# Kernel optimization log

Measured on AMD Instinct MI355X. Metric: run time of the kernel, lower is better.

The kernel has to match this reference:

```python
import jax, jax.numpy as jnp
import numpy as np

N_NODES = 100000
N_EDGES = 1600000
IN_F, HID, OUT_F = 128, 128, 64
BN_EPS = 1e-5


def _sage_conv(x, src, dst, W_l, b_l, W_r, n_nodes):
    # PyG SAGEConv (aggr='mean', root_weight=True):
    #   out_i = W_l @ mean_{j in N(i)} x_j + b_l + W_r @ x_i
    msg = x[src]                                             # [E, d] gather
    agg = jax.ops.segment_sum(msg, dst, num_segments=n_nodes)  # [N, d]
    deg = jax.ops.segment_sum(jnp.ones((src.shape[0],), x.dtype), dst,
                              num_segments=n_nodes)          # [N]
    agg = agg / jnp.clip(deg, 1.0)[:, None]
    return agg @ W_l.T + b_l + x @ W_r.T


def setup_inputs() -> dict:
    key = jax.random.key(0)
    ks = jax.random.split(key, 10)
    x = jax.random.normal(ks[0], (N_NODES, IN_F), dtype=jnp.float32)
    edge_index = jax.random.randint(ks[1], (2, N_EDGES), 0, N_NODES, dtype=jnp.int64)
    s = 0.05
    return {
        "x": x,
        "edge_index": edge_index,
        "W1_l": jax.random.normal(ks[2], (HID, IN_F), dtype=jnp.float32) * s,
        "b1": jnp.zeros((HID,), jnp.float32),
        "W1_r": jax.random.normal(ks[3], (HID, IN_F), dtype=jnp.float32) * s,
        "bn_gamma": jnp.ones((HID,), jnp.float32),
        "bn_beta": jnp.zeros((HID,), jnp.float32),
        "bn_mean": jax.random.normal(ks[4], (HID,), dtype=jnp.float32) * 0.1,
        "bn_var": jnp.ones((HID,), jnp.float32),
        "W2_l": jax.random.normal(ks[5], (OUT_F, HID), dtype=jnp.float32) * s,
        "b2": jnp.zeros((OUT_F,), jnp.float32),
        "W2_r": jax.random.normal(ks[6], (OUT_F, HID), dtype=jnp.float32) * s,
    }


def reference(x, edge_index, W1_l, b1, W1_r, bn_gamma, bn_beta, bn_mean, bn_var,
              W2_l, b2, W2_r):
    src, dst = edge_index[0], edge_index[1]
    n = x.shape[0]
    # eval mode: dropout = identity
    h = _sage_conv(x, src, dst, W1_l, b1, W1_r, n)            # [N, HID]
    # BatchNorm1d (eval, running stats)
    h = (h - bn_mean) * jax.lax.rsqrt(bn_var + BN_EPS) * bn_gamma + bn_beta
    h = jax.nn.relu(h)
    return _sage_conv(h, src, dst, W2_l, b2, W2_r, n)         # [N, OUT_F]
```

## Files before the change

### kernel.cpp

```cpp
#include <hip/hip_runtime.h>

#define FEAT 128
#define BN_EPS 1e-5f
#define CSTRIDE 16

typedef __attribute__((ext_vector_type(8))) short s8frag;
typedef __attribute__((ext_vector_type(4))) float f4frag;

union FragU { uint4 u; s8frag v; };

__device__ __forceinline__ unsigned short f2bf(float f) {
    unsigned u = __float_as_uint(f);
    unsigned r = (u + 0x7fffu + ((u >> 16) & 1u)) >> 16;
    return (unsigned short)r;
}
__device__ __forceinline__ void unpack2(unsigned d, float& lo, float& hi) {
    lo = __uint_as_float(d << 16);
    hi = __uint_as_float(d & 0xffff0000u);
}
__device__ __forceinline__ void acc8(float* acc, uint4 d) {
    float l, h;
    unpack2(d.x, l, h); acc[0] += l; acc[1] += h;
    unpack2(d.y, l, h); acc[2] += l; acc[3] += h;
    unpack2(d.z, l, h); acc[4] += l; acc[5] += h;
    unpack2(d.w, l, h); acc[6] += l; acc[7] += h;
}

__global__ __launch_bounds__(256) void front_kernel(
    const int* __restrict__ dst, int E, int Tc,
    unsigned* __restrict__ degc, unsigned char* __restrict__ rank8,
    const float* __restrict__ x, unsigned short* __restrict__ xb, int total8,
    const float* __restrict__ W1l, const float* __restrict__ W1r,
    const float* __restrict__ W2l, const float* __restrict__ W2r,
    const float* __restrict__ b1, const float* __restrict__ g,
    const float* __restrict__ bt, const float* __restrict__ mu,
    const float* __restrict__ var, const float* __restrict__ b2,
    unsigned short* __restrict__ Wb1, unsigned short* __restrict__ Wb2,
    float* __restrict__ bnsc, float* __restrict__ bnsh, float* __restrict__ cb2)
{
    int tid = blockIdx.x * 256 + threadIdx.x;
    if (tid < Tc) {
        int base = tid * 8;
        if (base + 8 <= E) {
            int4 d0 = *(const int4*)(dst + base);
            int4 d1 = *(const int4*)(dst + base + 4);
            unsigned r0 = atomicAdd(&degc[(size_t)d0.x * CSTRIDE], 1u);
            unsigned r1 = atomicAdd(&degc[(size_t)d0.y * CSTRIDE], 1u);
            unsigned r2 = atomicAdd(&degc[(size_t)d0.z * CSTRIDE], 1u);
            unsigned r3 = atomicAdd(&degc[(size_t)d0.w * CSTRIDE], 1u);
            unsigned r4 = atomicAdd(&degc[(size_t)d1.x * CSTRIDE], 1u);
            unsigned r5 = atomicAdd(&degc[(size_t)d1.y * CSTRIDE], 1u);
            unsigned r6 = atomicAdd(&degc[(size_t)d1.z * CSTRIDE], 1u);
            unsigned r7 = atomicAdd(&degc[(size_t)d1.w * CSTRIDE], 1u);
            unsigned p0 = (r0 & 255u) | ((r1 & 255u) << 8) | ((r2 & 255u) << 16) | ((r3 & 255u) << 24);
            unsigned p1 = (r4 & 255u) | ((r5 & 255u) << 8) | ((r6 & 255u) << 16) | ((r7 & 255u) << 24);
            ((unsigned*)rank8)[tid * 2]     = p0;
            ((unsigned*)rank8)[tid * 2 + 1] = p1;
        } else {
            for (int e = base; e < E; e++)
                rank8[e] = (unsigned char)atomicAdd(&degc[(size_t)dst[e] * CSTRIDE], 1u);
        }
    } else if (tid < Tc + total8) {
        int t = tid - Tc;
        const float4* src = (const float4*)(x) + (size_t)t * 2;
        float4 a = src[0], b = src[1];
        uint4 o;
        o.x = f2bf(a.x) | ((unsigned)f2bf(a.y) << 16);
        o.y = f2bf(a.z) | ((unsigned)f2bf(a.w) << 16);
        o.z = f2bf(b.x) | ((unsigned)f2bf(b.y) << 16);
        o.w = f2bf(b.z) | ((unsigned)f2bf(b.w) << 16);
        ((uint4*)xb)[t] = o;
    } else {
        int idx = tid - Tc - total8;
        if (idx < 128 * 256) {
            int n = idx >> 8, k = idx & 255;
            float w = (k < 128) ? W1l[n * 128 + k] : W1r[n * 128 + (k - 128)];
            Wb1[idx] = f2bf(w);
        }
        if (idx < 128 * 128) {
            int n = idx >> 7, k = idx & 127;
            float w = (n < 64) ? W2l[n * 128 + k] : W2r[(n - 64) * 128 + k];
            Wb2[idx] = f2bf(w);
        }
        if (idx < 128) {
            float sc = rsqrtf(var[idx] + BN_EPS) * g[idx];
            bnsc[idx] = sc;
            bnsh[idx] = sc * (b1[idx] - mu[idx]) + bt[idx];
            cb2[idx] = (idx < 64) ? 0.f : b2[idx - 64];
        }
    }
}

__global__ void scan_block(const unsigned* __restrict__ degc, unsigned* __restrict__ excl,
                           unsigned* __restrict__ partials, int N) {
    __shared__ unsigned buf[256];
    int i = blockIdx.x * 256 + threadIdx.x;
    unsigned v = (i < N) ? degc[(size_t)i * CSTRIDE] : 0u;
    buf[threadIdx.x] = v;
    __syncthreads();
    for (int off = 1; off < 256; off <<= 1) {
        unsigned t = (threadIdx.x >= (unsigned)off) ? buf[threadIdx.x - off] : 0u;
        __syncthreads();
        buf[threadIdx.x] += t;
        __syncthreads();
    }
    if (i < N) excl[i] = buf[threadIdx.x] - v;
    if (threadIdx.x == 255) partials[blockIdx.x] = buf[255];
}

__global__ void scan_finish(unsigned* __restrict__ row_start,
                            const unsigned* __restrict__ partials, int N, int E) {
    __shared__ unsigned red[256];
    int b = blockIdx.x;
    unsigned s = 0;
    for (int t = threadIdx.x; t < b; t += 256) s += partials[t];
    red[threadIdx.x] = s;
    __syncthreads();
    for (int off = 128; off > 0; off >>= 1) {
        if ((int)threadIdx.x < off) red[threadIdx.x] += red[threadIdx.x + off];
        __syncthreads();
    }
    unsigned base = red[0];
    int i = b * 256 + threadIdx.x;
    if (i < N) row_start[i] += base;
    if (i == 0) row_start[N] = (unsigned)E;
}

__global__ void fill_csr(const int* __restrict__ src, const int* __restrict__ dst, int E,
                         const unsigned* __restrict__ row_start,
                         const unsigned char* __restrict__ rank8,
                         unsigned* __restrict__ csr_src) {
    int base = (blockIdx.x * blockDim.x + threadIdx.x) * 4;
    if (base + 4 <= E) {
        int4 d = *(const int4*)(dst + base);
        int4 s = *(const int4*)(src + base);
        unsigned rp = ((const unsigned*)rank8)[base >> 2];
        unsigned p0 = row_start[d.x] + (rp & 255u);
        unsigned p1 = row_start[d.y] + ((rp >> 8) & 255u);
        unsigned p2 = row_start[d.z] + ((rp >> 16) & 255u);
        unsigned p3 = row_start[d.w] + ((rp >> 24) & 255u);
        csr_src[p0] = (unsigned)s.x;
        csr_src[p1] = (unsigned)s.y;
        csr_src[p2] = (unsigned)s.z;
        csr_src[p3] = (unsigned)s.w;
    } else {
        for (int e = base; e < E; e++)
            csr_src[row_start[dst[e]] + rank8[e]] = (unsigned)src[e];
    }
}

__global__ __launch_bounds__(256) void gather_mean_bf(const unsigned short* __restrict__ xb,
                                                      const unsigned* __restrict__ row_start,
                                                      const unsigned* __restrict__ csr_src,
                                                      unsigned short* __restrict__ aggb, int N) {
    int gid = blockIdx.x * 256 + threadIdx.x;
    int node = gid >> 4;
    if (node >= N) return;
    int f = (threadIdx.x & 15) * 8;
    unsigned s0 = row_start[node], s1 = row_start[node + 1];
    float acc[8];
#pragma unroll
    for (int i = 0; i < 8; i++) acc[i] = 0.f;
    unsigned i = s0;
    for (; i + 4 <= s1; i += 4) {
        unsigned sa = csr_src[i], sb = csr_src[i + 1];
        unsigned sc = csr_src[i + 2], sd = csr_src[i + 3];
        uint4 da = *(const uint4*)(xb + (size_t)sa * 128 + f);
        uint4 db = *(const uint4*)(xb + (size_t)sb * 128 + f);
        uint4 dc = *(const uint4*)(xb + (size_t)sc * 128 + f);
        uint4 dd = *(const uint4*)(xb + (size_t)sd * 128 + f);
        acc8(acc, da); acc8(acc, db); acc8(acc, dc); acc8(acc, dd);
    }
    for (; i < s1; i++) {
        unsigned sa = csr_src[i];
        uint4 da = *(const uint4*)(xb + (size_t)sa * 128 + f);
        acc8(acc, da);
    }
    float inv = (s1 > s0) ? 1.0f / (float)(s1 - s0) : 0.f;
    uint4 o;
    o.x = f2bf(acc[0] * inv) | ((unsigned)f2bf(acc[1] * inv) << 16);
    o.y = f2bf(acc[2] * inv) | ((unsigned)f2bf(acc[3] * inv) << 16);
    o.z = f2bf(acc[4] * inv) | ((unsigned)f2bf(acc[5] * inv) << 16);
    o.w = f2bf(acc[6] * inv) | ((unsigned)f2bf(acc[7] * inv) << 16);
    *(uint4*)(aggb + (size_t)node * 128 + f) = o;
}

__global__ __launch_bounds__(256) void sage_dense(
    const unsigned short* __restrict__ aggb,
    const unsigned short* __restrict__ xb,
    const unsigned short* __restrict__ Wb1,
    const unsigned short* __restrict__ Wb2,
    const float* __restrict__ bnsc, const float* __restrict__ bnsh,
    const float* __restrict__ cb2,
    unsigned short* __restrict__ uvb, int N)
{
    __shared__ __align__(16) unsigned short As[64 * 128];
    __shared__ __align__(16) unsigned short Bs[128 * 128];
    uint4* AsV = (uint4*)As;
    uint4* BsV = (uint4*)Bs;

    const int tid = threadIdx.x;
    const int wave = tid >> 6;
    const int lane = tid & 63;
    const int mr = lane & 15;
    const int q = lane >> 4;
    const int m0 = blockIdx.x * 64;
    const int mw = m0 + wave * 16 + mr;
    const bool mv = mw < N;

    FragU ag[4], ax[4];
#pragma unroll
    for (int kc4 = 0; kc4 < 4; kc4++) {
        ag[kc4].u = make_uint4(0u, 0u, 0u, 0u);
        ax[kc4].u = make_uint4(0u, 0u, 0u, 0u);
        if (mv) {
            ag[kc4].u = *(const uint4*)(aggb + (size_t)mw * 128 + kc4 * 32 + q * 8);
            ax[kc4].u = *(const uint4*)(xb + (size_t)mw * 128 + kc4 * 32 + q * 8);
        }
    }

#pragma unroll
    for (int i = 0; i < 8; i++) {
        int gch = tid + i * 256;
        int n = gch >> 4, c = gch & 15;
        BsV[n * 16 + (c ^ (n & 15))] = *(const uint4*)(Wb1 + (size_t)n * 256 + c * 8);
    }
    __syncthreads();

    f4frag acc[8];
#pragma unroll
    for (int j = 0; j < 8; j++)
#pragma unroll
        for (int r = 0; r < 4; r++) acc[j][r] = 0.f;

#pragma unroll
    for (int kc4 = 0; kc4 < 4; kc4++) {
#pragma unroll
        for (int j = 0; j < 8; j++) {
            FragU b;
            b.u = BsV[(j * 16 + mr) * 16 + ((kc4 * 4 + q) ^ mr)];
            acc[j] = __builtin_amdgcn_mfma_f32_16x16x32_bf16(ag[kc4].v, b.v, acc[j], 0, 0, 0);
        }
    }
    __syncthreads();

#pragma unroll
    for (int i = 0; i < 8; i++) {
        int gch = tid + i * 256;
        int n = gch >> 4, c = gch & 15;
        BsV[n * 16 + (c ^ (n & 15))] = *(const uint4*)(Wb1 + (size_t)n * 256 + 128 + c * 8);
    }
    __syncthreads();

#pragma unroll
    for (int kc4 = 0; kc4 < 4; kc4++) {
#pragma unroll
        for (int j = 0; j < 8; j++) {
            FragU b;
            b.u = BsV[(j * 16 + mr) * 16 + ((kc4 * 4 + q) ^ mr)];
            acc[j] = __builtin_amdgcn_mfma_f32_16x16x32_bf16(ax[kc4].v, b.v, acc[j], 0, 0, 0);
        }
    }

#pragma unroll
    for (int j = 0; j < 8; j++) {
        int n = j * 16 + mr;
        float sc = bnsc[n], sh = bnsh[n];
        int cn = n >> 3;
#pragma unroll
        for (int r = 0; r < 4; r++) {
            int ml = wave * 16 + q * 4 + r;
            float v = fmaxf(acc[j][r] * sc + sh, 0.f);
            As[(ml * 16 + (cn ^ (ml & 15))) * 8 + (n & 7)] = f2bf(v);
        }
    }
    __syncthreads();

#pragma unroll
    for (int i = 0; i < 8; i++) {
        int gch = tid + i * 256;
        int n = gch >> 4, c = gch & 15;
        BsV[n * 16 + (c ^ (n & 15))] = *(const uint4*)(Wb2 + (size_t)n * 128 + c * 8);
    }
    __syncthreads();

#pragma unroll
    for (int j = 0; j < 8; j++)
#pragma unroll
        for (int r = 0; r < 4; r++) acc[j][r] = 0.f;
    const int arow = (wave * 16 + mr) * 16;
#pragma unroll
    for (int kc4 = 0; kc4 < 4; kc4++) {
        FragU a;
        a.u = AsV[arow + ((kc4 * 4 + q) ^ mr)];
#pragma unroll
        for (int j = 0; j < 8; j++) {
            FragU b;
            b.u = BsV[(j * 16 + mr) * 16 + ((kc4 * 4 + q) ^ mr)];
            acc[j] = __builtin_amdgcn_mfma_f32_16x16x32_bf16(a.v, b.v, acc[j], 0, 0, 0);
        }
    }

#pragma unroll
    for (int j = 0; j < 8; j++) {
        int n = j * 16 + mr;
        float cb = cb2[n];
#pragma unroll
        for (int r = 0; r < 4; r++) {
            int mrow = m0 + wave * 16 + q * 4 + r;
            if (mrow < N)
                uvb[(size_t)mrow * 128 + n] = f2bf(acc[j][r] + cb);
        }
    }
}

__global__ __launch_bounds__(256) void gather_out_bf(const unsigned short* __restrict__ uvb,
                                                     const unsigned* __restrict__ row_start,
                                                     const unsigned* __restrict__ csr_src,
                                                     float* __restrict__ out, int N) {
    int gid = blockIdx.x * 256 + threadIdx.x;
    int node = gid >> 3;
    if (node >= N) return;
    int f = (threadIdx.x & 7) * 8;
    unsigned s0 = row_start[node], s1 = row_start[node + 1];
    float acc[8];
#pragma unroll
    for (int i = 0; i < 8; i++) acc[i] = 0.f;
    unsigned i = s0;
    for (; i + 4 <= s1; i += 4) {
        unsigned sa = csr_src[i], sb = csr_src[i + 1];
        unsigned sc = csr_src[i + 2], sd = csr_src[i + 3];
        uint4 da = *(const uint4*)(uvb + (size_t)sa * 128 + f);
        uint4 db = *(const uint4*)(uvb + (size_t)sb * 128 + f);
        uint4 dc = *(const uint4*)(uvb + (size_t)sc * 128 + f);
        uint4 dd = *(const uint4*)(uvb + (size_t)sd * 128 + f);
        acc8(acc, da); acc8(acc, db); acc8(acc, dc); acc8(acc, dd);
    }
    for (; i < s1; i++) {
        unsigned sa = csr_src[i];
        uint4 da = *(const uint4*)(uvb + (size_t)sa * 128 + f);
        acc8(acc, da);
    }
    float inv = (s1 > s0) ? 1.0f / (float)(s1 - s0) : 0.f;
    uint4 dv = *(const uint4*)(uvb + (size_t)node * 128 + 64 + f);
    float vv[8];
    unpack2(dv.x, vv[0], vv[1]);
    unpack2(dv.y, vv[2], vv[3]);
    unpack2(dv.z, vv[4], vv[5]);
    unpack2(dv.w, vv[6], vv[7]);
    float4 o0 = make_float4(acc[0] * inv + vv[0], acc[1] * inv + vv[1],
                            acc[2] * inv + vv[2], acc[3] * inv + vv[3]);
    float4 o1 = make_float4(acc[4] * inv + vv[4], acc[5] * inv + vv[5],
                            acc[6] * inv + vv[6], acc[7] * inv + vv[7]);
    *(float4*)(out + (size_t)node * 64 + f) = o0;
    *(float4*)(out + (size_t)node * 64 + f + 4) = o1;
}

extern "C" void kernel_launch(void* const* d_in, const int* in_sizes, int n_in,
                              void* d_out, int out_size, void* d_ws, size_t ws_size,
                              hipStream_t stream) {
    const float* x     = (const float*)d_in[0];
    const int*   edge  = (const int*)d_in[1];
    const float* W1l   = (const float*)d_in[2];
    const float* b1    = (const float*)d_in[3];
    const float* W1r   = (const float*)d_in[4];
    const float* gamma = (const float*)d_in[5];
    const float* beta  = (const float*)d_in[6];
    const float* mean  = (const float*)d_in[7];
    const float* var   = (const float*)d_in[8];
    const float* W2l   = (const float*)d_in[9];
    const float* b2    = (const float*)d_in[10];
    const float* W2r   = (const float*)d_in[11];

    const int N = in_sizes[0] / FEAT;
    const int E = in_sizes[1] / 2;
    const int* srcI = edge;
    const int* dstI = edge + E;

    unsigned short* uvb  = (unsigned short*)d_ws;
    unsigned short* aggb = uvb + (size_t)N * 128;
    unsigned short* xb   = aggb + (size_t)N * 128;
    unsigned short* Wb1  = xb + (size_t)N * 128;
    unsigned short* Wb2  = Wb1 + 256 * 128;
    float* bnsc = (float*)(Wb2 + 128 * 128);
    float* bnsh = bnsc + 128;
    float* cb2  = bnsh + 128;
    unsigned* degc      = (unsigned*)(cb2 + 128);
    unsigned* row_start = degc + (size_t)N * CSTRIDE;
    unsigned* partials  = row_start + (N + 1);
    unsigned char* rank8 = (unsigned char*)(partials + 1024);
    unsigned* csr_src   = (unsigned*)(rank8 + ((E + 3) & ~3));

    float* outp = (float*)d_out;
    const int nb = (N + 255) / 256;

    hipMemsetAsync(degc, 0, (size_t)N * CSTRIDE * sizeof(unsigned), stream);

    {
        const int Tc = (E + 7) / 8;
        const int total8 = N * FEAT / 8;
        const int prepT = 128 * 256;
        const int threads = Tc + total8 + prepT;
        front_kernel<<<(threads + 255) / 256, 256, 0, stream>>>(
            dstI, E, Tc, degc, rank8, x, xb, total8,
            W1l, W1r, W2l, W2r, b1, gamma, beta, mean, var, b2,
            Wb1, Wb2, bnsc, bnsh, cb2);
    }
    scan_block<<<nb, 256, 0, stream>>>(degc, row_start, partials, N);
    scan_finish<<<nb, 256, 0, stream>>>(row_start, partials, N, E);
    {
        int threads4 = (E + 3) / 4;
        fill_csr<<<(threads4 + 255) / 256, 256, 0, stream>>>(srcI, dstI, E, row_start, rank8, csr_src);
    }

    gather_mean_bf<<<(N * 16 + 255) / 256, 256, 0, stream>>>(xb, row_start, csr_src, aggb, N);
    sage_dense<<<(N + 63) / 64, 256, 0, stream>>>(aggb, xb, Wb1, Wb2, bnsc, bnsh, cb2, uvb, N);
    gather_out_bf<<<(N * 8 + 255) / 256, 256, 0, stream>>>(uvb, row_start, csr_src, outp, N);
}
```

Before: 335.9 us.

## Build CSR via two-level bucketed counting sort instead of global atomics

Replaces the global-atomic degree count, rank bytes and scatter fill with a partitioned counting sort. Edges are first histogrammed per 512-node bucket in shared memory, then scanned, scattered into buckets packed as src<<9 | local dst, and sorted within each bucket by a per-bucket block using shared-memory atomics. The aim is to remove scattered global atomics, the padded degree memset and random CSR writes. In exchange it adds an extra pass over the edge list and an intermediate buffer. It also requires src < 2^23 and at most 256 buckets.

```diff
diff --git a/kernel.cpp b/kernel.cpp
--- a/kernel.cpp
+++ b/kernel.cpp
@@ -2,7 +2,9 @@
 
 #define FEAT 128
 #define BN_EPS 1e-5f
-#define CSTRIDE 16
+#define P_CNT 1024
+#define BKT_SHIFT 9
+#define BKT_NODES 512
 
 typedef __attribute__((ext_vector_type(8))) short s8frag;
 typedef __attribute__((ext_vector_type(4))) float f4frag;
@@ -26,10 +28,10 @@
     unpack2(d.w, l, h); acc[6] += l; acc[7] += h;
 }
 
-__global__ __launch_bounds__(256) void front_kernel(
-    const int* __restrict__ dst, int E, int Tc,
-    unsigned* __restrict__ degc, unsigned char* __restrict__ rank8,
-    const float* __restrict__ x, unsigned short* __restrict__ xb, int total8,
+__global__ __launch_bounds__(256) void front2(
+    const int* __restrict__ dst, int E, int per, int NB,
+    unsigned* __restrict__ histT,
+    const float* __restrict__ x, unsigned short* __restrict__ xb, int XB,
     const float* __restrict__ W1l, const float* __restrict__ W1r,
     const float* __restrict__ W2l, const float* __restrict__ W2r,
     const float* __restrict__ b1, const float* __restrict__ g,
@@ -38,30 +40,21 @@
     unsigned short* __restrict__ Wb1, unsigned short* __restrict__ Wb2,
     float* __restrict__ bnsc, float* __restrict__ bnsh, float* __restrict__ cb2)
 {
-    int tid = blockIdx.x * 256 + threadIdx.x;
-    if (tid < Tc) {
-        int base = tid * 8;
-        if (base + 8 <= E) {
-            int4 d0 = *(const int4*)(dst + base);
-            int4 d1 = *(const int4*)(dst + base + 4);
-            unsigned r0 = atomicAdd(&degc[(size_t)d0.x * CSTRIDE], 1u);
-            unsigned r1 = atomicAdd(&degc[(size_t)d0.y * CSTRIDE], 1u);
-            unsigned r2 = atomicAdd(&degc[(size_t)d0.z * CSTRIDE], 1u);
-            unsigned r3 = atomicAdd(&degc[(size_t)d0.w * CSTRIDE], 1u);
-            unsigned r4 = atomicAdd(&degc[(size_t)d1.x * CSTRIDE], 1u);
-            unsigned r5 = atomicAdd(&degc[(size_t)d1.y * CSTRIDE], 1u);
-            unsigned r6 = atomicAdd(&degc[(size_t)d1.z * CSTRIDE], 1u);
-            unsigned r7 = atomicAdd(&degc[(size_t)d1.w * CSTRIDE], 1u);
-            unsigned p0 = (r0 & 255u) | ((r1 & 255u) << 8) | ((r2 & 255u) << 16) | ((r3 & 255u) << 24);
-            unsigned p1 = (r4 & 255u) | ((r5 & 255u) << 8) | ((r6 & 255u) << 16) | ((r7 & 255u) << 24);
-            ((unsigned*)rank8)[tid * 2]     = p0;
-            ((unsigned*)rank8)[tid * 2 + 1] = p1;
-        } else {
-            for (int e = base; e < E; e++)
-                rank8[e] = (unsigned char)atomicAdd(&degc[(size_t)dst[e] * CSTRIDE], 1u);
-        }
-    } else if (tid < Tc + total8) {
-        int t = tid - Tc;
+    const int bid = blockIdx.x;
+    const int tid = threadIdx.x;
+    if (bid < P_CNT) {
+        __shared__ unsigned h[256];
+        for (int i = tid; i < NB; i += 256) h[i] = 0u;
+        __syncthreads();
+        int s = bid * per;
+        int e1 = min(E, s + per);
+        for (int e = s + tid; e < e1; e += 256)
+            atomicAdd(&h[((unsigned)dst[e]) >> BKT_SHIFT], 1u);
+        __syncthreads();
+        for (int i = tid; i < NB; i += 256)
+            histT[(size_t)i * P_CNT + bid] = h[i];
+    } else if (bid < P_CNT + XB) {
+        int t = (bid - P_CNT) * 256 + tid;
         const float4* src = (const float4*)(x) + (size_t)t * 2;
         float4 a = src[0], b = src[1];
         uint4 o;
@@ -71,7 +64,7 @@
         o.w = f2bf(b.z) | ((unsigned)f2bf(b.w) << 16);
         ((uint4*)xb)[t] = o;
     } else {
-        int idx = tid - Tc - total8;
+        int idx = (bid - P_CNT - XB) * 256 + tid;
         if (idx < 128 * 256) {
             int n = idx >> 8, k = idx & 255;
             float w = (k < 128) ? W1l[n * 128 + k] : W1r[n * 128 + (k - 128)];
@@ -91,11 +84,11 @@
     }
 }
 
-__global__ void scan_block(const unsigned* __restrict__ degc, unsigned* __restrict__ excl,
-                           unsigned* __restrict__ partials, int N) {
+__global__ void scan_block_c(const unsigned* __restrict__ in, unsigned* __restrict__ excl,
+                             unsigned* __restrict__ partials, int M) {
     __shared__ unsigned buf[256];
     int i = blockIdx.x * 256 + threadIdx.x;
-    unsigned v = (i < N) ? degc[(size_t)i * CSTRIDE] : 0u;
+    unsigned v = (i < M) ? in[i] : 0u;
     buf[threadIdx.x] = v;
     __syncthreads();
     for (int off = 1; off < 256; off <<= 1) {
@@ -104,12 +97,12 @@
         buf[threadIdx.x] += t;
         __syncthreads();
     }
-    if (i < N) excl[i] = buf[threadIdx.x] - v;
+    if (i < M) excl[i] = buf[threadIdx.x] - v;
     if (threadIdx.x == 255) partials[blockIdx.x] = buf[255];
 }
 
-__global__ void scan_finish(unsigned* __restrict__ row_start,
-                            const unsigned* __restrict__ partials, int N, int E) {
+__global__ void scan_finish(unsigned* __restrict__ arr,
+                            const unsigned* __restrict__ partials, int M, int E) {
     __shared__ unsigned red[256];
     int b = blockIdx.x;
     unsigned s = 0;
@@ -122,31 +115,60 @@
     }
     unsigned base = red[0];
     int i = b * 256 + threadIdx.x;
-    if (i < N) row_start[i] += base;
-    if (i == 0) row_start[N] = (unsigned)E;
-}
-
-__global__ void fill_csr(const int* __restrict__ src, const int* __restrict__ dst, int E,
-                         const unsigned* __restrict__ row_start,
-                         const unsigned char* __restrict__ rank8,
-                         unsigned* __restrict__ csr_src) {
-    int base = (blockIdx.x * blockDim.x + threadIdx.x) * 4;
-    if (base + 4 <= E) {
-        int4 d = *(const int4*)(dst + base);
-        int4 s = *(const int4*)(src + base);
-        unsigned rp = ((const unsigned*)rank8)[base >> 2];
-        unsigned p0 = row_start[d.x] + (rp & 255u);
-        unsigned p1 = row_start[d.y] + ((rp >> 8) & 255u);
-        unsigned p2 = row_start[d.z] + ((rp >> 16) & 255u);
-        unsigned p3 = row_start[d.w] + ((rp >> 24) & 255u);
-        csr_src[p0] = (unsigned)s.x;
-        csr_src[p1] = (unsigned)s.y;
-        csr_src[p2] = (unsigned)s.z;
-        csr_src[p3] = (unsigned)s.w;
-    } else {
-        for (int e = base; e < E; e++)
-            csr_src[row_start[dst[e]] + rank8[e]] = (unsigned)src[e];
-    }
+    if (i < M) arr[i] += base;
+    if (i == 0) arr[M] = (unsigned)E;
+}
+
+__global__ __launch_bounds__(256) void scatter_bucket(
+    const int* __restrict__ src, const int* __restrict__ dst, int E, int per, int NB,
+    const unsigned* __restrict__ hexcl, unsigned* __restrict__ buck)
+{
+    __shared__ unsigned cnt[256];
+    const int p = blockIdx.x, tid = threadIdx.x;
+    for (int i = tid; i < NB; i += 256) cnt[i] = hexcl[(size_t)i * P_CNT + p];
+    __syncthreads();
+    int s = p * per, e1 = min(E, s + per);
+    for (int e = s + tid; e < e1; e += 256) {
+        unsigned d = (unsigned)dst[e];
+        unsigned pos = atomicAdd(&cnt[d >> BKT_SHIFT], 1u);
+        buck[pos] = ((unsigned)src[e] << BKT_SHIFT) | (d & (BKT_NODES - 1u));
+    }
+}
+
+__global__ __launch_bounds__(512) void bucket_csr(
+    const unsigned* __restrict__ buck, const unsigned* __restrict__ hexcl,
+    unsigned* __restrict__ row_start, unsigned* __restrict__ csr_src, int N, int E)
+{
+    __shared__ unsigned h[BKT_NODES];
+    __shared__ unsigned sc[BKT_NODES];
+    const int b = blockIdx.x, tid = threadIdx.x;
+    const unsigned bs = hexcl[(size_t)b * P_CNT];
+    const unsigned be = hexcl[(size_t)(b + 1) * P_CNT];
+    h[tid] = 0u;
+    __syncthreads();
+    for (unsigned e = bs + tid; e < be; e += BKT_NODES)
+        atomicAdd(&h[buck[e] & (BKT_NODES - 1u)], 1u);
+    __syncthreads();
+    unsigned v = h[tid];
+    sc[tid] = v;
+    __syncthreads();
+    for (int off = 1; off < BKT_NODES; off <<= 1) {
+        unsigned t = (tid >= off) ? sc[tid - off] : 0u;
+        __syncthreads();
+        sc[tid] += t;
+        __syncthreads();
+    }
+    unsigned pos0 = bs + sc[tid] - v;
+    int node = b * BKT_NODES + tid;
+    if (node < N) row_start[node] = pos0;
+    h[tid] = pos0;
+    __syncthreads();
+    for (unsigned e = bs + tid; e < be; e += BKT_NODES) {
+        unsigned pk = buck[e];
+        unsigned pos = atomicAdd(&h[pk & (BKT_NODES - 1u)], 1u);
+        csr_src[pos] = pk >> BKT_SHIFT;
+    }
+    if (b == 0 && tid == 0) row_start[N] = (unsigned)E;
 }
 
 __global__ __launch_bounds__(256) void gather_mean_bf(const unsigned short* __restrict__ xb,
@@ -377,6 +399,10 @@
     const int* srcI = edge;
     const int* dstI = edge + E;
 
+    const int NB  = (N + BKT_NODES - 1) >> BKT_SHIFT;
+    const int M   = NB * P_CNT;
+    const int per = (E + P_CNT - 1) / P_CNT;
+
     unsigned short* uvb  = (unsigned short*)d_ws;
     unsigned short* aggb = uvb + (size_t)N * 128;
     unsigned short* xb   = aggb + (size_t)N * 128;
@@ -385,33 +411,27 @@
     float* bnsc = (float*)(Wb2 + 128 * 128);
     float* bnsh = bnsc + 128;
     float* cb2  = bnsh + 128;
-    unsigned* degc      = (unsigned*)(cb2 + 128);
-    unsigned* row_start = degc + (size_t)N * CSTRIDE;
-    unsigned* partials  = row_start + (N + 1);
-    unsigned char* rank8 = (unsigned char*)(partials + 1024);
-    unsigned* csr_src   = (unsigned*)(rank8 + ((E + 3) & ~3));
+    unsigned* histT     = (unsigned*)(cb2 + 128);
+    unsigned* hexcl     = histT + (M + 1);
+    unsigned* partials  = hexcl + (M + 1);
+    unsigned* row_start = partials + 1024;
+    unsigned* buck      = row_start + (N + 1);
+    unsigned* csr_src   = buck + E;
 
     float* outp = (float*)d_out;
-    const int nb = (N + 255) / 256;
-
-    hipMemsetAsync(degc, 0, (size_t)N * CSTRIDE * sizeof(unsigned), stream);
-
-    {
-        const int Tc = (E + 7) / 8;
-        const int total8 = N * FEAT / 8;
-        const int prepT = 128 * 256;
-        const int threads = Tc + total8 + prepT;
-        front_kernel<<<(threads + 255) / 256, 256, 0, stream>>>(
-            dstI, E, Tc, degc, rank8, x, xb, total8,
-            W1l, W1r, W2l, W2r, b1, gamma, beta, mean, var, b2,
-            Wb1, Wb2, bnsc, bnsh, cb2);
-    }
-    scan_block<<<nb, 256, 0, stream>>>(degc, row_start, partials, N);
-    scan_finish<<<nb, 256, 0, stream>>>(row_start, partials, N, E);
-    {
-        int threads4 = (E + 3) / 4;
-        fill_csr<<<(threads4 + 255) / 256, 256, 0, stream>>>(srcI, dstI, E, row_start, rank8, csr_src);
-    }
+
+    const int total8 = N * FEAT / 8;
+    const int XB = (total8 + 255) / 256;
+    const int PB = (128 * 256 + 255) / 256;
+    front2<<<P_CNT + XB + PB, 256, 0, stream>>>(
+        dstI, E, per, NB, histT, x, xb, XB,
+        W1l, W1r, W2l, W2r, b1, gamma, beta, mean, var, b2,
+        Wb1, Wb2, bnsc, bnsh, cb2);
+
+    scan_block_c<<<M / 256, 256, 0, stream>>>(histT, hexcl, partials, M);
+    scan_finish<<<M / 256, 256, 0, stream>>>(hexcl, partials, M, E);
+    scatter_bucket<<<P_CNT, 256, 0, stream>>>(srcI, dstI, E, per, NB, hexcl, buck);
+    bucket_csr<<<NB, BKT_NODES, 0, stream>>>(buck, hexcl, row_start, csr_src, N, E);
 
     gather_mean_bf<<<(N * 16 + 255) / 256, 256, 0, stream>>>(xb, row_start, csr_src, aggb, N);
     sage_dense<<<(N + 63) / 64, 256, 0, stream>>>(aggb, xb, Wb1, Wb2, bnsc, bnsh, cb2, uvb, N);
```

Result: faster. 286.6 us (-14.7%).
